# Optimization experiments

Measured on AMD Instinct MI355X. Metric: run time of the kernel, lower is better.

The kernel has to match this reference:

```python
import jax, jax.numpy as jnp
import numpy as np

EPS = 1e-08
ITERATIONS = 3


def squash(s):
    # s: [..., d]
    s2 = jnp.sum(s * s, axis=-1, keepdims=True)
    return s2 / (1.0 + s2) * (s / jnp.sqrt(s2 + EPS))


def setup_inputs() -> dict:
    key = jax.random.key(0)
    k1, k2 = jax.random.split(key)
    B, IN_CAPS, OUT_CAPS, IN_D, OUT_D = 256, 1152, 10, 8, 16
    u = jax.random.normal(k1, (B, IN_CAPS, IN_D), dtype=jnp.float32)
    weight = jax.random.normal(k2, (IN_CAPS, OUT_CAPS, IN_D, OUT_D), dtype=jnp.float32)
    return {"u": u, "weight": weight}


def reference(u, weight):
    # u: [B, in_caps, in_d]; weight: [in_caps, out_caps, in_d, out_d]
    u_hat = jnp.einsum('ijnm,bin->bijm', weight, u)  # [B, in_caps, out_caps, out_d]
    B, in_caps, out_caps, _ = u_hat.shape
    b = jnp.zeros((B, in_caps, out_caps), dtype=u.dtype)
    v = None
    for _ in range(ITERATIONS):
        c = jax.nn.softmax(b, axis=1)  # softmax over in_caps (dim=1, faithful to source)
        s = jnp.einsum('bij,bijm->bjm', c, u_hat)  # [B, out_caps, out_d]
        v = squash(s)
        a = jnp.einsum('bjm,bijm->bij', v, u_hat)
        b = b + a
    return v
```

## Files before the change

### kernel.cpp

```cpp
#include <hip/hip_runtime.h>
#include <hip/hip_bf16.h>
#include <math.h>


#define IC 1152
#define OC 10
#define NB 256
#define TILE_DW (IC * 8)

typedef float v2f __attribute__((ext_vector_type(2)));

__device__ __forceinline__ float bf_lo(unsigned w) { return __uint_as_float(w << 16); }
__device__ __forceinline__ float bf_hi(unsigned w) { return __uint_as_float(w & 0xFFFF0000u); }
__device__ __forceinline__ v2f bf_v2(unsigned w) {
    v2f r = { __uint_as_float(w << 16), __uint_as_float(w & 0xFFFF0000u) };
    return r;
}
__device__ __forceinline__ unsigned pack2(float a, float b) {
    __hip_bfloat162 h = __float22bfloat162_rn(make_float2(a, b));
    return *(unsigned*)&h;
}
__device__ __forceinline__ unsigned short pack1(float a) {
    __hip_bfloat16 h = __float2bfloat16(a);
    return *(unsigned short*)&h;
}

__global__ __launch_bounds__(512, 4)
void caps_route_kernel(const float* __restrict__ u,
                       const float* __restrict__ W,
                       float* __restrict__ out) {
    extern __shared__ unsigned smem_u[];
    unsigned* uh = smem_u;
    unsigned short* ce = (unsigned short*)(uh + 2 * TILE_DW);
    float* spart = (float*)(ce + 2 * IC);

    const int t    = threadIdx.x;
    const int bx   = blockIdx.x;
    const int lane = t & 63;
    const int wid  = t >> 6;

    int x = bx & 7, sg = bx >> 3;
    int j, p;
    if (sg < 128) { j = x; p = sg; }
    else { int s2 = sg - 128; j = 8 + (x >> 2); p = ((x & 3) << 5) + s2; }
    const int bb = p * 2;

    {
        const int q  = t & 3;
        const int i0 = t >> 2;
        const int pb = (((q >> 1) ^ ((i0 >> 2) & 1)) << 2) + ((q & 1) << 1);
        const float* u0p = u + (size_t)bb * (IC * 8);
#pragma unroll 3
        for (int k = 0; k < 9; ++k) {
            const int i = i0 + 128 * k;
            const float4* wrow = (const float4*)(W + ((size_t)(i * OC + j) << 7)) + q;
            const float4 ua0 = *(const float4*)(u0p + i * 8);
            const float4 ua1 = *(const float4*)(u0p + i * 8 + 4);
            const float4 ub0 = *(const float4*)(u0p + IC * 8 + i * 8);
            const float4 ub1 = *(const float4*)(u0p + IC * 8 + i * 8 + 4);
            v2f a01 = {0.f,0.f}, a23 = {0.f,0.f};
            v2f b01 = {0.f,0.f}, b23 = {0.f,0.f};
#define ST(ux, uy, n) {                                                   \
            const float4 w4 = wrow[(n) * 4];                              \
            const v2f w01 = {w4.x, w4.y}, w23 = {w4.z, w4.w};             \
            const v2f us = {(ux), (ux)}, vs = {(uy), (uy)};               \
            a01 += us * w01; a23 += us * w23;                             \
            b01 += vs * w01; b23 += vs * w23; }
            ST(ua0.x, ub0.x, 0) ST(ua0.y, ub0.y, 1) ST(ua0.z, ub0.z, 2) ST(ua0.w, ub0.w, 3)
            ST(ua1.x, ub1.x, 4) ST(ua1.y, ub1.y, 5) ST(ua1.z, ub1.z, 6) ST(ua1.w, ub1.w, 7)
#undef ST
            const int dst = (i << 3) + pb;
            *(uint2*)&uh[dst]           = make_uint2(pack2(a01.x, a01.y), pack2(a23.x, a23.y));
            *(uint2*)&uh[TILE_DW + dst] = make_uint2(pack2(b01.x, b01.y), pack2(b23.x, b23.y));
        }
    }

    __syncthreads();

    if (wid >= 6) {
        __syncthreads();
        __syncthreads();
        __syncthreads();
        return;
    }

    const int bt = (wid >= 3) ? 1 : 0;
    const int w3 = wid - bt * 3;
    const int rowbase = w3 * 384;
    const unsigned* uhT = uh + bt * TILE_DW;
    unsigned short* ceT = ce + bt * IC;
    float* spB[2] = { spart + bt * 60, spart + 120 + bt * 60 };

    const int mqc = lane & 3;
    const int h   = lane >> 2;
    const int pbS = (((mqc >> 1) ^ ((h >> 2) & 1)) << 2) + ((mqc & 1) << 1);
    const bool eB = ((lane >> 2) & 1) != 0;

    float L[6];
#pragma unroll
    for (int k = 0; k < 6; ++k) L[k] = 0.f;
    float se = 0.f;
    float4 acc, vq;

    for (int r = 0; r < 3; ++r) {
        v2f aA = {0.f, 0.f}, aB = {0.f, 0.f};
        if (r == 0) {
#pragma unroll 6
            for (int k = 0; k < 24; ++k) {
                const int i = rowbase + 16 * k + h;
                const uint2 d = *(const uint2*)&uhT[(i << 3) + pbS];
                aA += bf_v2(d.x);
                aB += bf_v2(d.y);
            }
        } else {
#pragma unroll 6
            for (int k = 0; k < 24; ++k) {
                const int i = rowbase + 16 * k + h;
                const uint2 d = *(const uint2*)&uhT[(i << 3) + pbS];
                const float c = __uint_as_float(((unsigned)ceT[i]) << 16);
                const v2f cs = {c, c};
                aA += cs * bf_v2(d.x);
                aB += cs * bf_v2(d.y);
            }
        }
        acc = make_float4(aA.x, aA.y, aB.x, aB.y);
#pragma unroll
        for (int o = 4; o <= 32; o <<= 1) {
            acc.x += __shfl_xor(acc.x, o, 64); acc.y += __shfl_xor(acc.y, o, 64);
            acc.z += __shfl_xor(acc.z, o, 64); acc.w += __shfl_xor(acc.w, o, 64);
        }
        float* sp = spB[r & 1];
        if (lane < 4) *(float4*)&sp[w3 * 20 + (lane << 2)] = acc;
        else if (r > 0 && lane == 4) sp[w3 * 20 + 16] = se;
        __syncthreads();

        {
            const int o1 = ((w3 + 1) % 3) * 20, o2 = ((w3 + 2) % 3) * 20;
            const float4 q1 = *(const float4*)&sp[o1 + (mqc << 2)];
            const float4 q2 = *(const float4*)&sp[o2 + (mqc << 2)];
            const float inv = (r == 0) ? (1.0f / (float)IC)
                                       : 1.0f / (se + sp[o1 + 16] + sp[o2 + 16]);
            const float4 s4 = make_float4((acc.x + q1.x + q2.x) * inv,
                                          (acc.y + q1.y + q2.y) * inv,
                                          (acc.z + q1.z + q2.z) * inv,
                                          (acc.w + q1.w + q2.w) * inv);
            float p2 = s4.x*s4.x + s4.y*s4.y + s4.z*s4.z + s4.w*s4.w;
            p2 += __shfl_xor(p2, 1, 64);
            p2 += __shfl_xor(p2, 2, 64);
            const float sc = p2 / ((1.0f + p2) * sqrtf(p2 + 1e-8f));
            vq = make_float4(s4.x * sc, s4.y * sc, s4.z * sc, s4.w * sc);
        }

        if (r == 2) {
            if (w3 == 0 && lane < 4)
                *(float4*)&out[((size_t)(bb + bt) * OC + j) * 16 + (lane << 2)] = vq;
        } else {
            const float4 q0 = make_float4(__shfl(vq.x,0,4), __shfl(vq.y,0,4),
                                          __shfl(vq.z,0,4), __shfl(vq.w,0,4));
            const float4 q1 = make_float4(__shfl(vq.x,1,4), __shfl(vq.y,1,4),
                                          __shfl(vq.z,1,4), __shfl(vq.w,1,4));
            const float4 q2 = make_float4(__shfl(vq.x,2,4), __shfl(vq.y,2,4),
                                          __shfl(vq.z,2,4), __shfl(vq.w,2,4));
            const float4 q3 = make_float4(__shfl(vq.x,3,4), __shfl(vq.y,3,4),
                                          __shfl(vq.z,3,4), __shfl(vq.w,3,4));
            const float4 Qa0 = eB ? q2 : q0, Qa1 = eB ? q3 : q1;
            const float4 Qb0 = eB ? q0 : q2, Qb1 = eB ? q1 : q3;
            const v2f va0 = {Qa0.x, Qa0.y}, va1 = {Qa0.z, Qa0.w};
            const v2f va2 = {Qa1.x, Qa1.y}, va3 = {Qa1.z, Qa1.w};
            const v2f vb0 = {Qb0.x, Qb0.y}, vb1 = {Qb0.z, Qb0.w};
            const v2f vb2 = {Qb1.x, Qb1.y}, vb3 = {Qb1.z, Qb1.w};
            se = 0.f;
#pragma unroll 3
            for (int k = 0; k < 6; ++k) {
                const int i = rowbase + lane + 64 * k;
                const uint4 da = *(const uint4*)&uhT[i << 3];
                const uint4 db = *(const uint4*)&uhT[(i << 3) + 4];
                v2f dp = {0.f, 0.f};
                dp += bf_v2(da.x) * va0;
                dp += bf_v2(da.y) * va1;
                dp += bf_v2(da.z) * va2;
                dp += bf_v2(da.w) * va3;
                dp += bf_v2(db.x) * vb0;
                dp += bf_v2(db.y) * vb1;
                dp += bf_v2(db.z) * vb2;
                dp += bf_v2(db.w) * vb3;
                L[k] += dp.x + dp.y;
                const float ev = __expf(L[k]);
                ceT[i] = pack1(ev);
                se += ev;
            }
#pragma unroll
            for (int o = 32; o >= 1; o >>= 1) se += __shfl_xor(se, o, 64);
        }
    }
}

extern "C" void kernel_launch(void* const* d_in, const int* in_sizes, int n_in,
                              void* d_out, int out_size, void* d_ws, size_t ws_size,
                              hipStream_t stream) {
    const float* u = (const float*)d_in[0];
    const float* W = (const float*)d_in[1];
    float* out = (float*)d_out;

    const size_t shmem = (size_t)2 * TILE_DW * 4
                       + (size_t)2 * IC * 2
                       + 240 * 4;
    hipFuncSetAttribute((const void*)caps_route_kernel,
                        hipFuncAttributeMaxDynamicSharedMemorySize, (int)shmem);

    caps_route_kernel<<<(NB / 2) * OC, 512, shmem, stream>>>(u, W, out);
}
```

Before: 125.2 us.

## Double block size to 1024 threads and split routing across six waves per batch

Doubles the block from 512 to 1024 threads. The u_hat staging loop now covers rows with a 256-row stride plus a tail step. Routing now uses six waves per batch element instead of three, each handling 192 rows, and the partial-sum reduction buffer is widened to hold six partials. The aim is to cut the serial per-thread work in staging and routing by adding parallelism. In exchange, 1024-thread blocks with about 78KB of LDS each allow fewer blocks per CU, and the cross-wave reduction gets larger.

```diff
diff --git a/kernel.cpp b/kernel.cpp
--- a/kernel.cpp
+++ b/kernel.cpp
@@ -10,8 +10,6 @@
 
 typedef float v2f __attribute__((ext_vector_type(2)));
 
-__device__ __forceinline__ float bf_lo(unsigned w) { return __uint_as_float(w << 16); }
-__device__ __forceinline__ float bf_hi(unsigned w) { return __uint_as_float(w & 0xFFFF0000u); }
 __device__ __forceinline__ v2f bf_v2(unsigned w) {
     v2f r = { __uint_as_float(w << 16), __uint_as_float(w & 0xFFFF0000u) };
     return r;
@@ -25,7 +23,7 @@
     return *(unsigned short*)&h;
 }
 
-__global__ __launch_bounds__(512, 4)
+__global__ __launch_bounds__(1024, 4)
 void caps_route_kernel(const float* __restrict__ u,
                        const float* __restrict__ W,
                        float* __restrict__ out) {
@@ -50,9 +48,8 @@
         const int i0 = t >> 2;
         const int pb = (((q >> 1) ^ ((i0 >> 2) & 1)) << 2) + ((q & 1) << 1);
         const float* u0p = u + (size_t)bb * (IC * 8);
-#pragma unroll 3
-        for (int k = 0; k < 9; ++k) {
-            const int i = i0 + 128 * k;
+
+        auto stage = [&](int i) {
             const float4* wrow = (const float4*)(W + ((size_t)(i * OC + j) << 7)) + q;
             const float4 ua0 = *(const float4*)(u0p + i * 8);
             const float4 ua1 = *(const float4*)(u0p + i * 8 + 4);
@@ -72,41 +69,43 @@
             const int dst = (i << 3) + pb;
             *(uint2*)&uh[dst]           = make_uint2(pack2(a01.x, a01.y), pack2(a23.x, a23.y));
             *(uint2*)&uh[TILE_DW + dst] = make_uint2(pack2(b01.x, b01.y), pack2(b23.x, b23.y));
-        }
+        };
+#pragma unroll
+        for (int k = 0; k < 4; ++k) stage(i0 + 256 * k);
+        if (i0 < IC - 1024) stage(i0 + 1024);
     }
 
     __syncthreads();
 
-    if (wid >= 6) {
+    if (wid >= 12) {
         __syncthreads();
         __syncthreads();
         __syncthreads();
         return;
     }
 
-    const int bt = (wid >= 3) ? 1 : 0;
-    const int w3 = wid - bt * 3;
-    const int rowbase = w3 * 384;
+    const int bt = (wid >= 6) ? 1 : 0;
+    const int w6 = wid - bt * 6;
+    const int rowbase = w6 * 192;
     const unsigned* uhT = uh + bt * TILE_DW;
     unsigned short* ceT = ce + bt * IC;
-    float* spB[2] = { spart + bt * 60, spart + 120 + bt * 60 };
 
     const int mqc = lane & 3;
     const int h   = lane >> 2;
     const int pbS = (((mqc >> 1) ^ ((h >> 2) & 1)) << 2) + ((mqc & 1) << 1);
     const bool eB = ((lane >> 2) & 1) != 0;
 
-    float L[6];
-#pragma unroll
-    for (int k = 0; k < 6; ++k) L[k] = 0.f;
+    float L[3];
+#pragma unroll
+    for (int k = 0; k < 3; ++k) L[k] = 0.f;
     float se = 0.f;
-    float4 acc, vq;
+    float4 vq;
 
     for (int r = 0; r < 3; ++r) {
         v2f aA = {0.f, 0.f}, aB = {0.f, 0.f};
         if (r == 0) {
 #pragma unroll 6
-            for (int k = 0; k < 24; ++k) {
+            for (int k = 0; k < 12; ++k) {
                 const int i = rowbase + 16 * k + h;
                 const uint2 d = *(const uint2*)&uhT[(i << 3) + pbS];
                 aA += bf_v2(d.x);
@@ -114,7 +113,7 @@
             }
         } else {
 #pragma unroll 6
-            for (int k = 0; k < 24; ++k) {
+            for (int k = 0; k < 12; ++k) {
                 const int i = rowbase + 16 * k + h;
                 const uint2 d = *(const uint2*)&uhT[(i << 3) + pbS];
                 const float c = __uint_as_float(((unsigned)ceT[i]) << 16);
@@ -123,27 +122,28 @@
                 aB += cs * bf_v2(d.y);
             }
         }
-        acc = make_float4(aA.x, aA.y, aB.x, aB.y);
+        float4 acc = make_float4(aA.x, aA.y, aB.x, aB.y);
 #pragma unroll
         for (int o = 4; o <= 32; o <<= 1) {
             acc.x += __shfl_xor(acc.x, o, 64); acc.y += __shfl_xor(acc.y, o, 64);
             acc.z += __shfl_xor(acc.z, o, 64); acc.w += __shfl_xor(acc.w, o, 64);
         }
-        float* sp = spB[r & 1];
-        if (lane < 4) *(float4*)&sp[w3 * 20 + (lane << 2)] = acc;
-        else if (r > 0 && lane == 4) sp[w3 * 20 + 16] = se;
+        float* spR = spart + (r & 1) * 240 + bt * 120;
+        if (lane < 4) *(float4*)&spR[w6 * 20 + (lane << 2)] = acc;
+        else if (r > 0 && lane == 4) spR[w6 * 20 + 16] = se;
         __syncthreads();
 
         {
-            const int o1 = ((w3 + 1) % 3) * 20, o2 = ((w3 + 2) % 3) * 20;
-            const float4 q1 = *(const float4*)&sp[o1 + (mqc << 2)];
-            const float4 q2 = *(const float4*)&sp[o2 + (mqc << 2)];
-            const float inv = (r == 0) ? (1.0f / (float)IC)
-                                       : 1.0f / (se + sp[o1 + 16] + sp[o2 + 16]);
-            const float4 s4 = make_float4((acc.x + q1.x + q2.x) * inv,
-                                          (acc.y + q1.y + q2.y) * inv,
-                                          (acc.z + q1.z + q2.z) * inv,
-                                          (acc.w + q1.w + q2.w) * inv);
+            float4 ss = {0.f, 0.f, 0.f, 0.f};
+            float sesum = 0.f;
+#pragma unroll
+            for (int s6 = 0; s6 < 6; ++s6) {
+                const float4 qq = *(const float4*)&spR[s6 * 20 + (mqc << 2)];
+                ss.x += qq.x; ss.y += qq.y; ss.z += qq.z; ss.w += qq.w;
+                sesum += spR[s6 * 20 + 16];
+            }
+            const float inv = (r == 0) ? (1.0f / (float)IC) : 1.0f / sesum;
+            const float4 s4 = make_float4(ss.x * inv, ss.y * inv, ss.z * inv, ss.w * inv);
             float p2 = s4.x*s4.x + s4.y*s4.y + s4.z*s4.z + s4.w*s4.w;
             p2 += __shfl_xor(p2, 1, 64);
             p2 += __shfl_xor(p2, 2, 64);
@@ -152,7 +152,7 @@
         }
 
         if (r == 2) {
-            if (w3 == 0 && lane < 4)
+            if (w6 == 0 && lane < 4)
                 *(float4*)&out[((size_t)(bb + bt) * OC + j) * 16 + (lane << 2)] = vq;
         } else {
             const float4 q0 = make_float4(__shfl(vq.x,0,4), __shfl(vq.y,0,4),
@@ -170,8 +170,8 @@
             const v2f vb0 = {Qb0.x, Qb0.y}, vb1 = {Qb0.z, Qb0.w};
             const v2f vb2 = {Qb1.x, Qb1.y}, vb3 = {Qb1.z, Qb1.w};
             se = 0.f;
-#pragma unroll 3
-            for (int k = 0; k < 6; ++k) {
+#pragma unroll
+            for (int k = 0; k < 3; ++k) {
                 const int i = rowbase + lane + 64 * k;
                 const uint4 da = *(const uint4*)&uhT[i << 3];
                 const uint4 db = *(const uint4*)&uhT[(i << 3) + 4];
@@ -204,9 +204,9 @@
 
     const size_t shmem = (size_t)2 * TILE_DW * 4
                        + (size_t)2 * IC * 2
-                       + 240 * 4;
+                       + 480 * 4;
     hipFuncSetAttribute((const void*)caps_route_kernel,
                         hipFuncAttributeMaxDynamicSharedMemorySize, (int)shmem);
 
-    caps_route_kernel<<<(NB / 2) * OC, 512, shmem, stream>>>(u, W, out);
-}
+    caps_route_kernel<<<(NB / 2) * OC, 1024, shmem, stream>>>(u, W, out);
+}
```

New measurement: 120.4 us. 3.8% less time.
